# Kernel optimization log

Measured on AMD Instinct MI355X. Metric: run time of the kernel, lower is better.

The kernel has to match this reference:

```python
import jax, jax.numpy as jnp
import numpy as np

TOP_K = 4


def setup_inputs() -> dict:
    key = jax.random.key(0)
    k1, k2, k3 = jax.random.split(key, 3)
    T, H, E = 16384, 2880, 128
    hidden_states = jax.random.normal(k1, (T, H), dtype=jnp.float32)
    weight = jax.random.normal(k2, (E, H), dtype=jnp.float32) * 0.02
    bias = jax.random.normal(k3, (E,), dtype=jnp.float32) * 0.02
    return {"hidden_states": hidden_states, "weight": weight, "bias": bias}


def reference(hidden_states, weight, bias):
    # [T, H] @ [H, E] + [E] -> router logits [T, E]
    hidden_states = hidden_states.reshape(-1, weight.shape[1])
    router_logits = jnp.einsum('th,eh->te', hidden_states, weight) + bias
    # top-k over experts, then softmax over the k selected logits
    router_top_value, router_indices = jax.lax.top_k(router_logits, TOP_K)
    router_scores = jax.nn.softmax(router_top_value, axis=-1)
    return router_scores, router_indices
```

## Files before the change

### kernel.cpp

```cpp
#include <hip/hip_runtime.h>
#include <hip/hip_bf16.h>
#include <math.h>

#define T_TOKENS 16384
#define H_DIM    2880
#define KHALF    1440
#define E_EXP    128
#define TOPK     4
#define MT       32
#define MTM      64
#define KC       32
#define NCHUNK   (H_DIM / KC)
#define NCHUNK_H (KHALF / KC)
#define EPS_GAP  5e-4f

#define WS_WOFF   64
#define WS_WBYTES (NCHUNK * 1024 * 16)
#define WS_FLOFF  (WS_WOFF + WS_WBYTES)
#define WS_NEED   (WS_FLOFF + T_TOKENS * 4)

typedef __bf16 bf16x8 __attribute__((ext_vector_type(8)));
typedef float  f32x4  __attribute__((ext_vector_type(4)));

__device__ __forceinline__ void split2(float a, float b,
                                       unsigned int& hi, unsigned int& lo) {
    float2 p; p.x = a; p.y = b;
    __hip_bfloat162 h = __float22bfloat162_rn(p);
    unsigned int hu; __builtin_memcpy(&hu, &h, 4);
    float2 r;
    r.x = a - __uint_as_float((hu & 0xffffu) << 16);
    r.y = b - __uint_as_float(hu & 0xffff0000u);
    __hip_bfloat162 l = __float22bfloat162_rn(r);
    unsigned int lu; __builtin_memcpy(&lu, &l, 4);
    hi = hu; lo = lu;
}

__global__ __launch_bounds__(256) void prep_w(const float* __restrict__ W,
                                              uint4* __restrict__ wsW) {
    const int f   = blockIdx.x * 256 + threadIdx.x;
    const int kc  = f >> 9;
    const int rem = f & 511;
    const int nt  = rem >> 6;
    const int L   = rem & 63;
    const int e   = nt * 16 + (L & 15);
    const int k   = kc * KC + (L >> 4) * 8;
    const float* p = W + (size_t)e * H_DIM + k;
    const float4 x0 = *(const float4*)p;
    const float4 x1 = *(const float4*)(p + 4);
    uint4 hi, lo;
    split2(x0.x, x0.y, hi.x, lo.x);
    split2(x0.z, x0.w, hi.y, lo.y);
    split2(x1.x, x1.y, hi.z, lo.z);
    split2(x1.z, x1.w, hi.w, lo.w);
    wsW[(size_t)kc * 1024 + nt * 64 + L]       = hi;
    wsW[(size_t)kc * 1024 + 512 + nt * 64 + L] = lo;
}

__global__ __launch_bounds__(1024, 4) void router_main(
    const float* __restrict__ A, const uint4* __restrict__ wsW,
    const float* __restrict__ bias, float* __restrict__ out,
    int* __restrict__ flag_count, int* __restrict__ flag_list)
{
    union SMem {
        struct {
            uint4 W  [2][2][1024];
            uint4 Ahi[2][2][4][64];
            uint4 Alo[2][2][4][64];
        } s;
        float L[MTM][129];
    };
    __shared__ SMem sm;

    const int tid    = threadIdx.x;
    const int t_base = blockIdx.x * MTM;

    const int wave  = tid >> 6;
    const int L     = tid & 63;
    const int whalf = wave >> 3;
    const int wmg   = (wave >> 2) & 1;
    const int wng   = wave & 3;

    const int shalf = whalf;
    const int wv    = wave & 7;
    const uint4* wsrc = wsW + (size_t)(shalf * NCHUNK_H) * 1024 + (wv * 2) * 64 + L;

    const bool doA = tid < 512;
    const int at   = (tid >> 3) & 63;
    const int ac   = tid & 7;
    const int ah   = ac >> 2;
    const int akq  = ac & 3;
    const int awm  = at >> 4;
    const int aL   = (akq << 4) | (at & 15);
    const float* Ag = A + (size_t)(t_base + at) * H_DIM + ah * KHALF + akq * 8;

    f32x4 acc[2][2];
#pragma unroll
    for (int m = 0; m < 2; ++m)
#pragma unroll
        for (int n = 0; n < 2; ++n) { f32x4 z = {0.f, 0.f, 0.f, 0.f}; acc[m][n] = z; }

#define STAGE(NB, IT)                                                          \
    {                                                                          \
        if (doA) {                                                             \
            uint4 hi4, lo4;                                                    \
            split2(av0.x, av0.y, hi4.x, lo4.x);                                \
            split2(av0.z, av0.w, hi4.y, lo4.y);                                \
            split2(av1.x, av1.y, hi4.z, lo4.z);                                \
            split2(av1.z, av1.w, hi4.w, lo4.w);                                \
            sm.s.Ahi[NB][ah][awm][aL] = hi4;                                   \
            sm.s.Alo[NB][ah][awm][aL] = lo4;                                   \
        }                                                                      \
        const uint4* wc = wsrc + (size_t)(IT) * 1024;                          \
        _Pragma("unroll")                                                      \
        for (int j = 0; j < 2; ++j) {                                          \
            __builtin_amdgcn_global_load_lds(                                  \
                (const __attribute__((address_space(1))) void*)(wc + j * 64),  \
                (__attribute__((address_space(3))) void*)&sm.s.W[NB][shalf][(wv * 2 + j) * 64], \
                16, 0, 0);                                                     \
        }                                                                      \
    }

    float4 av0, av1;
    if (doA) { av0 = *(const float4*)(Ag); av1 = *(const float4*)(Ag + 4); }
    STAGE(0, 0);
    if (doA) { av0 = *(const float4*)(Ag + KC); av1 = *(const float4*)(Ag + KC + 4); }
    __syncthreads();

    int b = 0;
    for (int it = 0; it < NCHUNK_H; ++it) {
        if (it + 1 < NCHUNK_H) {
            STAGE(b ^ 1, it + 1);
            if (doA && it + 2 < NCHUNK_H) {
                av0 = *(const float4*)(Ag + (it + 2) * KC);
                av1 = *(const float4*)(Ag + (it + 2) * KC + 4);
            }
        }
        const bf16x8 ah0 = *(const bf16x8*)&sm.s.Ahi[b][whalf][wmg * 2 + 0][L];
        const bf16x8 al0 = *(const bf16x8*)&sm.s.Alo[b][whalf][wmg * 2 + 0][L];
        const bf16x8 ah1 = *(const bf16x8*)&sm.s.Ahi[b][whalf][wmg * 2 + 1][L];
        const bf16x8 al1 = *(const bf16x8*)&sm.s.Alo[b][whalf][wmg * 2 + 1][L];
#pragma unroll
        for (int n = 0; n < 2; ++n) {
            const int nt = wng * 2 + n;
            const bf16x8 whi = *(const bf16x8*)&sm.s.W[b][whalf][nt * 64 + L];
            const bf16x8 wlo = *(const bf16x8*)&sm.s.W[b][whalf][512 + nt * 64 + L];
            acc[0][n] = __builtin_amdgcn_mfma_f32_16x16x32_bf16(ah0, whi, acc[0][n], 0, 0, 0);
            acc[0][n] = __builtin_amdgcn_mfma_f32_16x16x32_bf16(ah0, wlo, acc[0][n], 0, 0, 0);
            acc[0][n] = __builtin_amdgcn_mfma_f32_16x16x32_bf16(al0, whi, acc[0][n], 0, 0, 0);
            acc[1][n] = __builtin_amdgcn_mfma_f32_16x16x32_bf16(ah1, whi, acc[1][n], 0, 0, 0);
            acc[1][n] = __builtin_amdgcn_mfma_f32_16x16x32_bf16(ah1, wlo, acc[1][n], 0, 0, 0);
            acc[1][n] = __builtin_amdgcn_mfma_f32_16x16x32_bf16(al1, whi, acc[1][n], 0, 0, 0);
        }
        __syncthreads();
        b ^= 1;
    }
#undef STAGE

    if (whalf == 0) {
#pragma unroll
        for (int m = 0; m < 2; ++m)
#pragma unroll
            for (int n = 0; n < 2; ++n) {
                const int e = (wng * 2 + n) * 16 + (L & 15);
                const float bv = bias[e];
#pragma unroll
                for (int r = 0; r < 4; ++r)
                    sm.L[(wmg * 2 + m) * 16 + (L >> 4) * 4 + r][e] = acc[m][n][r] + bv;
            }
    }
    __syncthreads();
    if (whalf == 1) {
#pragma unroll
        for (int m = 0; m < 2; ++m)
#pragma unroll
            for (int n = 0; n < 2; ++n) {
                const int e = (wng * 2 + n) * 16 + (L & 15);
#pragma unroll
                for (int r = 0; r < 4; ++r)
                    sm.L[(wmg * 2 + m) * 16 + (L >> 4) * 4 + r][e] += acc[m][n][r];
            }
    }
    __syncthreads();

    if (tid < MTM) {
        float v0 = -1e30f, v1 = -1e30f, v2 = -1e30f, v3 = -1e30f, v4 = -1e30f;
        int   i0 = 0, i1 = 0, i2 = 0, i3 = 0, i4 = 0;
        for (int e = 0; e < E_EXP; ++e) {
            const float x = sm.L[tid][e];
            if (x > v4) {
                if (x > v0)      { v4=v3;i4=i3; v3=v2;i3=i2; v2=v1;i2=i1; v1=v0;i1=i0; v0=x;i0=e; }
                else if (x > v1) { v4=v3;i4=i3; v3=v2;i3=i2; v2=v1;i2=i1; v1=x;i1=e; }
                else if (x > v2) { v4=v3;i4=i3; v3=v2;i3=i2; v2=x;i2=e; }
                else if (x > v3) { v4=v3;i4=i3; v3=x;i3=e; }
                else             { v4=x;i4=e; }
            }
        }
        const float g0 = v0 - v1, g1 = v1 - v2, g2 = v2 - v3, g3 = v3 - v4;
        float mg = g0 < g1 ? g0 : g1;
        mg = mg < g2 ? mg : g2;
        mg = mg < g3 ? mg : g3;

        const float e0x = expf(v0 - v0);
        const float e1x = expf(v1 - v0);
        const float e2x = expf(v2 - v0);
        const float e3x = expf(v3 - v0);
        const float s   = e0x + e1x + e2x + e3x;

        const int gt = t_base + tid;
        float* out_scores = out;
        float* out_idx    = out + (size_t)T_TOKENS * TOPK;
        out_scores[gt * 4 + 0] = e0x / s;
        out_scores[gt * 4 + 1] = e1x / s;
        out_scores[gt * 4 + 2] = e2x / s;
        out_scores[gt * 4 + 3] = e3x / s;
        out_idx[gt * 4 + 0] = (float)i0;
        out_idx[gt * 4 + 1] = (float)i1;
        out_idx[gt * 4 + 2] = (float)i2;
        out_idx[gt * 4 + 3] = (float)i3;

        if (mg < EPS_GAP) {
            const int p = atomicAdd(flag_count, 1);
            if (p < T_TOKENS) flag_list[p] = gt;
        }
    }
}

__global__ __launch_bounds__(512, 4) void router_main_fb(
    const float* __restrict__ A, const float* __restrict__ W,
    const float* __restrict__ bias, float* __restrict__ out,
    int* __restrict__ flag_count, int* __restrict__ flag_list)
{
    __shared__ __align__(16) uint2 sAhi[2][2][128];
    __shared__ __align__(16) uint2 sAlo[2][2][128];
    __shared__ __align__(16) uint4 sWhi[2][8][64];
    __shared__ __align__(16) uint4 sWlo[2][8][64];
    __shared__ float sL[MT][129];

    const int tid    = threadIdx.x;
    const int t_base = blockIdx.x * MT;
    const int wave  = tid >> 6;
    const int L     = tid & 63;
    const int whalf = wave >> 2;
    const int wm    = wave & 1;
    const int wn    = (wave >> 1) & 1;
    const int shalf = tid >> 8;
    const int tid_h = tid & 255;
    const int at = tid_h >> 3;
    const int ac = tid_h & 7;
    const int a_idx = (at >> 4) * 128 + ((((ac >> 1) << 4) | (at & 15)) << 1) + (ac & 1);
    const float* Ag = A + (size_t)(t_base + at) * H_DIM + shalf * KHALF + ac * 4;
    const int we  = tid_h >> 1;
    const int wq0 = (tid_h & 1) * 2;
    const float* Wg = W + (size_t)we * H_DIM + shalf * KHALF + wq0 * 8;
    const int w_nt = we >> 4;
    const int w_n  = we & 15;

    uint2* sAhiF = &sAhi[shalf][0][0];
    uint2* sAloF = &sAlo[shalf][0][0];

    f32x4 acc[4];
#pragma unroll
    for (int i = 0; i < 4; ++i) { f32x4 z = {0.f, 0.f, 0.f, 0.f}; acc[i] = z; }

    for (int k0 = 0; k0 < KHALF; k0 += KC) {
        const float4 av  = *(const float4*)(Ag + k0);
        const float4 wv0 = *(const float4*)(Wg + k0);
        const float4 wv1 = *(const float4*)(Wg + k0 + 4);
        const float4 wv2 = *(const float4*)(Wg + k0 + 8);
        const float4 wv3 = *(const float4*)(Wg + k0 + 12);

        uint2 ahp, alp;
        split2(av.x, av.y, ahp.x, alp.x);
        split2(av.z, av.w, ahp.y, alp.y);
        uint4 whp0, wlp0, whp1, wlp1;
        split2(wv0.x, wv0.y, whp0.x, wlp0.x);
        split2(wv0.z, wv0.w, whp0.y, wlp0.y);
        split2(wv1.x, wv1.y, whp0.z, wlp0.z);
        split2(wv1.z, wv1.w, whp0.w, wlp0.w);
        split2(wv2.x, wv2.y, whp1.x, wlp1.x);
        split2(wv2.z, wv2.w, whp1.y, wlp1.y);
        split2(wv3.x, wv3.y, whp1.z, wlp1.z);
        split2(wv3.z, wv3.w, whp1.w, wlp1.w);

        __syncthreads();
        sAhiF[a_idx] = ahp;
        sAloF[a_idx] = alp;
        sWhi[shalf][w_nt][((wq0 + 0) << 4) | w_n] = whp0;
        sWhi[shalf][w_nt][((wq0 + 1) << 4) | w_n] = whp1;
        sWlo[shalf][w_nt][((wq0 + 0) << 4) | w_n] = wlp0;
        sWlo[shalf][w_nt][((wq0 + 1) << 4) | w_n] = wlp1;
        __syncthreads();

        const bf16x8 ahi = *(const bf16x8*)&sAhi[whalf][wm][L * 2];
        const bf16x8 alo = *(const bf16x8*)&sAlo[whalf][wm][L * 2];
#pragma unroll
        for (int i = 0; i < 4; ++i) {
            const int nt = wn * 4 + i;
            const bf16x8 whi = *(const bf16x8*)&sWhi[whalf][nt][L];
            const bf16x8 wlo = *(const bf16x8*)&sWlo[whalf][nt][L];
            acc[i] = __builtin_amdgcn_mfma_f32_16x16x32_bf16(ahi, whi, acc[i], 0, 0, 0);
            acc[i] = __builtin_amdgcn_mfma_f32_16x16x32_bf16(ahi, wlo, acc[i], 0, 0, 0);
            acc[i] = __builtin_amdgcn_mfma_f32_16x16x32_bf16(alo, whi, acc[i], 0, 0, 0);
        }
    }

    __syncthreads();
    if (whalf == 0) {
#pragma unroll
        for (int i = 0; i < 4; ++i) {
            const int e = wn * 64 + i * 16 + (L & 15);
            const float b = bias[e];
#pragma unroll
            for (int r = 0; r < 4; ++r)
                sL[wm * 16 + (L >> 4) * 4 + r][e] = acc[i][r] + b;
        }
    }
    __syncthreads();
    if (whalf == 1) {
#pragma unroll
        for (int i = 0; i < 4; ++i) {
            const int e = wn * 64 + i * 16 + (L & 15);
#pragma unroll
            for (int r = 0; r < 4; ++r)
                sL[wm * 16 + (L >> 4) * 4 + r][e] += acc[i][r];
        }
    }
    __syncthreads();

    if (tid < MT) {
        float v0 = -1e30f, v1 = -1e30f, v2 = -1e30f, v3 = -1e30f, v4 = -1e30f;
        int   i0 = 0, i1 = 0, i2 = 0, i3 = 0, i4 = 0;
        for (int e = 0; e < E_EXP; ++e) {
            const float x = sL[tid][e];
            if (x > v4) {
                if (x > v0)      { v4=v3;i4=i3; v3=v2;i3=i2; v2=v1;i2=i1; v1=v0;i1=i0; v0=x;i0=e; }
                else if (x > v1) { v4=v3;i4=i3; v3=v2;i3=i2; v2=v1;i2=i1; v1=x;i1=e; }
                else if (x > v2) { v4=v3;i4=i3; v3=v2;i3=i2; v2=x;i2=e; }
                else if (x > v3) { v4=v3;i4=i3; v3=x;i3=e; }
                else             { v4=x;i4=e; }
            }
        }
        const float g0 = v0 - v1, g1 = v1 - v2, g2 = v2 - v3, g3 = v3 - v4;
        float mg = g0 < g1 ? g0 : g1;
        mg = mg < g2 ? mg : g2;
        mg = mg < g3 ? mg : g3;

        const float e0x = expf(v0 - v0);
        const float e1x = expf(v1 - v0);
        const float e2x = expf(v2 - v0);
        const float e3x = expf(v3 - v0);
        const float s   = e0x + e1x + e2x + e3x;

        const int gt = t_base + tid;
        float* out_scores = out;
        float* out_idx    = out + (size_t)T_TOKENS * TOPK;
        out_scores[gt * 4 + 0] = e0x / s;
        out_scores[gt * 4 + 1] = e1x / s;
        out_scores[gt * 4 + 2] = e2x / s;
        out_scores[gt * 4 + 3] = e3x / s;
        out_idx[gt * 4 + 0] = (float)i0;
        out_idx[gt * 4 + 1] = (float)i1;
        out_idx[gt * 4 + 2] = (float)i2;
        out_idx[gt * 4 + 3] = (float)i3;

        if (mg < EPS_GAP) {
            const int p = atomicAdd(flag_count, 1);
            if (p < T_TOKENS) flag_list[p] = gt;
        }
    }
}

__global__ __launch_bounds__(256) void router_recheck(
    const float* __restrict__ A, const float* __restrict__ W,
    const float* __restrict__ bias, float* __restrict__ out,
    const int* __restrict__ flag_count, const int* __restrict__ flag_list)
{
    __shared__ double sPart[256];
    __shared__ double sLog[E_EXP];

    int count = *flag_count;
    if (count > T_TOKENS) count = T_TOKENS;

    const int tid = threadIdx.x;
    const int e   = tid & (E_EXP - 1);
    const int h   = tid >> 7;

    for (int i = blockIdx.x; i < count; i += gridDim.x) {
        const int t = flag_list[i];
        const float* arow = A + (size_t)t * H_DIM + h * KHALF;
        const float* wrow = W + (size_t)e * H_DIM + h * KHALF;

        double s0 = 0.0, s1 = 0.0, s2 = 0.0, s3 = 0.0;
        float4 a[8], w[8];
#pragma unroll
        for (int q = 0; q < 8; ++q) {
            a[q] = *(const float4*)(arow + q * 4);
            w[q] = *(const float4*)(wrow + q * 4);
        }
        for (int it = 0; it < KHALF / 32 - 1; ++it) {
            const float* ap = arow + (it + 1) * 32;
            const float* wp = wrow + (it + 1) * 32;
            float4 na[8], nw[8];
#pragma unroll
            for (int q = 0; q < 8; ++q) {
                na[q] = *(const float4*)(ap + q * 4);
                nw[q] = *(const float4*)(wp + q * 4);
            }
#pragma unroll
            for (int q = 0; q < 8; ++q) {
                s0 += (double)a[q].x * (double)w[q].x;
                s1 += (double)a[q].y * (double)w[q].y;
                s2 += (double)a[q].z * (double)w[q].z;
                s3 += (double)a[q].w * (double)w[q].w;
            }
#pragma unroll
            for (int q = 0; q < 8; ++q) { a[q] = na[q]; w[q] = nw[q]; }
        }
#pragma unroll
        for (int q = 0; q < 8; ++q) {
            s0 += (double)a[q].x * (double)w[q].x;
            s1 += (double)a[q].y * (double)w[q].y;
            s2 += (double)a[q].z * (double)w[q].z;
            s3 += (double)a[q].w * (double)w[q].w;
        }
        sPart[tid] = (s0 + s1) + (s2 + s3);
        __syncthreads();
        if (h == 0) sLog[e] = sPart[e] + sPart[e + 128] + (double)bias[e];
        __syncthreads();

        if (tid == 0) {
            double v0 = -1e300, v1 = -1e300, v2 = -1e300, v3 = -1e300;
            int    i0 = 0, i1 = 0, i2 = 0, i3 = 0;
            for (int q = 0; q < E_EXP; ++q) {
                const double x = sLog[q];
                if (x > v3) {
                    if (x > v0)      { v3=v2;i3=i2; v2=v1;i2=i1; v1=v0;i1=i0; v0=x;i0=q; }
                    else if (x > v1) { v3=v2;i3=i2; v2=v1;i2=i1; v1=x;i1=q; }
                    else if (x > v2) { v3=v2;i3=i2; v2=x;i2=q; }
                    else             { v3=x;i3=q; }
                }
            }
            const double e0x = exp(v0 - v0);
            const double e1x = exp(v1 - v0);
            const double e2x = exp(v2 - v0);
            const double e3x = exp(v3 - v0);
            const double s   = e0x + e1x + e2x + e3x;
            float* out_scores = out;
            float* out_idx    = out + (size_t)T_TOKENS * TOPK;
            out_scores[t * 4 + 0] = (float)(e0x / s);
            out_scores[t * 4 + 1] = (float)(e1x / s);
            out_scores[t * 4 + 2] = (float)(e2x / s);
            out_scores[t * 4 + 3] = (float)(e3x / s);
            out_idx[t * 4 + 0] = (float)i0;
            out_idx[t * 4 + 1] = (float)i1;
            out_idx[t * 4 + 2] = (float)i2;
            out_idx[t * 4 + 3] = (float)i3;
        }
        __syncthreads();
    }
}

extern "C" void kernel_launch(void* const* d_in, const int* in_sizes, int n_in,
                              void* d_out, int out_size, void* d_ws, size_t ws_size,
                              hipStream_t stream) {
    const float* A    = (const float*)d_in[0];
    const float* W    = (const float*)d_in[1];
    const float* bias = (const float*)d_in[2];
    float* out = (float*)d_out;

    if (ws_size >= (size_t)WS_NEED) {
        int*  flag_count = (int*)d_ws;
        int*  flag_list  = (int*)((char*)d_ws + WS_FLOFF);
        uint4* wsW       = (uint4*)((char*)d_ws + WS_WOFF);
        hipMemsetAsync(flag_count, 0, sizeof(int), stream);
        prep_w<<<dim3((NCHUNK * 512) / 256), dim3(256), 0, stream>>>(W, wsW);
        router_main<<<dim3(T_TOKENS / MTM), dim3(1024), 0, stream>>>(A, wsW, bias, out,
                                                                     flag_count, flag_list);
        router_recheck<<<dim3(512), dim3(256), 0, stream>>>(A, W, bias, out,
                                                            flag_count, flag_list);
    } else {
        int* flag_count = (int*)d_ws;
        int* flag_list  = (int*)d_ws + 1;
        hipMemsetAsync(flag_count, 0, sizeof(int), stream);
        router_main_fb<<<dim3(T_TOKENS / MT), dim3(512), 0, stream>>>(A, W, bias, out,
                                                                      flag_count, flag_list);
        router_recheck<<<dim3(512), dim3(256), 0, stream>>>(A, W, bias, out,
                                                            flag_count, flag_list);
    }
}
```

Before: 374.5 us.

## Restrict fp64 recheck to near-threshold candidate experts and remap A staging

When the main kernel flags a token with a small top-k gap, it now records up to eight candidate experts whose logits lie within the gap tolerance of the fourth value. The recheck kernel then recomputes exact double-precision logits only for those candidates, and falls back to all 128 experts when there are more than eight. The token row is staged in shared memory once. The A-tile thread mapping in the main kernel is also changed so each wave writes contiguous LDS slots. The cost is a serial 128-element scan per flagged token in the main kernel's epilogue and extra workspace for the candidate list.

```diff
diff --git a/kernel.cpp b/kernel.cpp
--- a/kernel.cpp
+++ b/kernel.cpp
@@ -17,7 +17,8 @@
 #define WS_WOFF   64
 #define WS_WBYTES (NCHUNK * 1024 * 16)
 #define WS_FLOFF  (WS_WOFF + WS_WBYTES)
-#define WS_NEED   (WS_FLOFF + T_TOKENS * 4)
+#define WS_CAOFF  (WS_FLOFF + T_TOKENS * 4)
+#define WS_NEED   (WS_CAOFF + T_TOKENS * 8)
 
 typedef __bf16 bf16x8 __attribute__((ext_vector_type(8)));
 typedef float  f32x4  __attribute__((ext_vector_type(4)));
@@ -59,7 +60,8 @@
 __global__ __launch_bounds__(1024, 4) void router_main(
     const float* __restrict__ A, const uint4* __restrict__ wsW,
     const float* __restrict__ bias, float* __restrict__ out,
-    int* __restrict__ flag_count, int* __restrict__ flag_list)
+    int* __restrict__ flag_count, int* __restrict__ flag_list,
+    uint2* __restrict__ cand_list)
 {
     union SMem {
         struct {
@@ -85,12 +87,11 @@
     const uint4* wsrc = wsW + (size_t)(shalf * NCHUNK_H) * 1024 + (wv * 2) * 64 + L;
 
     const bool doA = tid < 512;
-    const int at   = (tid >> 3) & 63;
-    const int ac   = tid & 7;
-    const int ah   = ac >> 2;
-    const int akq  = ac & 3;
-    const int awm  = at >> 4;
-    const int aL   = (akq << 4) | (at & 15);
+    const int ah   = wave & 1;
+    const int awm  = (wave >> 1) & 3;
+    const int akq  = L >> 4;
+    const int t16  = L & 15;
+    const int at   = awm * 16 + t16;
     const float* Ag = A + (size_t)(t_base + at) * H_DIM + ah * KHALF + akq * 8;
 
     f32x4 acc[2][2];
@@ -107,8 +108,8 @@
             split2(av0.z, av0.w, hi4.y, lo4.y);                                \
             split2(av1.x, av1.y, hi4.z, lo4.z);                                \
             split2(av1.z, av1.w, hi4.w, lo4.w);                                \
-            sm.s.Ahi[NB][ah][awm][aL] = hi4;                                   \
-            sm.s.Alo[NB][ah][awm][aL] = lo4;                                   \
+            sm.s.Ahi[NB][ah][awm][L] = hi4;                                    \
+            sm.s.Alo[NB][ah][awm][L] = lo4;                                    \
         }                                                                      \
         const uint4* wc = wsrc + (size_t)(IT) * 1024;                          \
         _Pragma("unroll")                                                      \
@@ -220,8 +221,150 @@
 
         if (mg < EPS_GAP) {
             const int p = atomicAdd(flag_count, 1);
-            if (p < T_TOKENS) flag_list[p] = gt;
-        }
+            if (p < T_TOKENS) {
+                flag_list[p] = gt;
+                unsigned ids[8];
+                int nc = 0;
+                const float thr = v3 - EPS_GAP;
+                for (int e = 0; e < E_EXP; ++e) {
+                    if (sm.L[tid][e] >= thr) {
+                        if (nc < 8) ids[nc] = (unsigned)e;
+                        ++nc;
+                    }
+                }
+                uint2 cd;
+                if (nc > 8) {
+                    cd.x = 0xFEu; cd.y = 0xFFFFFFFFu;
+                } else {
+                    for (int q = nc; q < 8; ++q) ids[q] = 0xFFu;
+                    cd.x = ids[0] | (ids[1] << 8) | (ids[2] << 16) | (ids[3] << 24);
+                    cd.y = ids[4] | (ids[5] << 8) | (ids[6] << 16) | (ids[7] << 24);
+                }
+                cand_list[p] = cd;
+            }
+        }
+    }
+}
+
+__global__ __launch_bounds__(256) void router_recheck(
+    const float* __restrict__ A, const float* __restrict__ W,
+    const float* __restrict__ bias, float* __restrict__ out,
+    const int* __restrict__ flag_count, const int* __restrict__ flag_list,
+    const uint2* __restrict__ cand_list)
+{
+    __shared__ float  sA[H_DIM];
+    __shared__ double sLog[8];
+    __shared__ int    sIds[8];
+    __shared__ double sPart[256];
+    __shared__ double sFull[E_EXP];
+
+    int count = *flag_count;
+    if (count > T_TOKENS) count = T_TOKENS;
+
+    const int tid = threadIdx.x;
+
+    for (int i = blockIdx.x; i < count; i += gridDim.x) {
+        const int t = flag_list[i];
+        const uint2 cd = cand_list[i];
+        __syncthreads();
+
+        for (int q = tid; q < H_DIM / 4; q += 256)
+            *(float4*)&sA[q * 4] = *(const float4*)(A + (size_t)t * H_DIM + q * 4);
+        __syncthreads();
+
+        const bool full = ((cd.x & 0xFFu) == 0xFEu);
+        if (!full) {
+            const int sl = tid >> 5;
+            const int j  = tid & 31;
+            const unsigned e = (sl < 4 ? (cd.x >> (sl * 8)) : (cd.y >> ((sl - 4) * 8))) & 0xFFu;
+            double sum = 0.0;
+            if (e < E_EXP) {
+                const float* wrow = W + (size_t)e * H_DIM;
+                for (int k = j; k < H_DIM; k += 32)
+                    sum += (double)sA[k] * (double)wrow[k];
+            }
+#pragma unroll
+            for (int off = 16; off > 0; off >>= 1)
+                sum += __shfl_down(sum, off, 32);
+            if (j == 0) {
+                sIds[sl] = (e < E_EXP) ? (int)e : -1;
+                sLog[sl] = (e < E_EXP) ? (sum + (double)bias[e]) : -1e300;
+            }
+            __syncthreads();
+            if (tid == 0) {
+                double v0 = -1e300, v1 = -1e300, v2 = -1e300, v3 = -1e300;
+                int    i0 = 0, i1 = 0, i2 = 0, i3 = 0;
+                for (int q = 0; q < 8; ++q) {
+                    if (sIds[q] < 0) continue;
+                    const double x = sLog[q];
+                    const int    id = sIds[q];
+                    if (x > v3) {
+                        if (x > v0)      { v3=v2;i3=i2; v2=v1;i2=i1; v1=v0;i1=i0; v0=x;i0=id; }
+                        else if (x > v1) { v3=v2;i3=i2; v2=v1;i2=i1; v1=x;i1=id; }
+                        else if (x > v2) { v3=v2;i3=i2; v2=x;i2=id; }
+                        else             { v3=x;i3=id; }
+                    }
+                }
+                const double e0x = exp(v0 - v0);
+                const double e1x = exp(v1 - v0);
+                const double e2x = exp(v2 - v0);
+                const double e3x = exp(v3 - v0);
+                const double s   = e0x + e1x + e2x + e3x;
+                float* out_scores = out;
+                float* out_idx    = out + (size_t)T_TOKENS * TOPK;
+                out_scores[t * 4 + 0] = (float)(e0x / s);
+                out_scores[t * 4 + 1] = (float)(e1x / s);
+                out_scores[t * 4 + 2] = (float)(e2x / s);
+                out_scores[t * 4 + 3] = (float)(e3x / s);
+                out_idx[t * 4 + 0] = (float)i0;
+                out_idx[t * 4 + 1] = (float)i1;
+                out_idx[t * 4 + 2] = (float)i2;
+                out_idx[t * 4 + 3] = (float)i3;
+            }
+        } else {
+            const int e = tid & (E_EXP - 1);
+            const int h = tid >> 7;
+            const float* wrow = W + (size_t)e * H_DIM + h * KHALF;
+            const float* arow = &sA[h * KHALF];
+            double s0 = 0.0, s1 = 0.0;
+            for (int k = 0; k < KHALF; k += 2) {
+                s0 += (double)arow[k]     * (double)wrow[k];
+                s1 += (double)arow[k + 1] * (double)wrow[k + 1];
+            }
+            sPart[tid] = s0 + s1;
+            __syncthreads();
+            if (h == 0) sFull[e] = sPart[e] + sPart[e + 128] + (double)bias[e];
+            __syncthreads();
+            if (tid == 0) {
+                double v0 = -1e300, v1 = -1e300, v2 = -1e300, v3 = -1e300;
+                int    i0 = 0, i1 = 0, i2 = 0, i3 = 0;
+                for (int q = 0; q < E_EXP; ++q) {
+                    const double x = sFull[q];
+                    if (x > v3) {
+                        if (x > v0)      { v3=v2;i3=i2; v2=v1;i2=i1; v1=v0;i1=i0; v0=x;i0=q; }
+                        else if (x > v1) { v3=v2;i3=i2; v2=v1;i2=i1; v1=x;i1=q; }
+                        else if (x > v2) { v3=v2;i3=i2; v2=x;i2=q; }
+                        else             { v3=x;i3=q; }
+                    }
+                }
+                const double e0x = exp(v0 - v0);
+                const double e1x = exp(v1 - v0);
+                const double e2x = exp(v2 - v0);
+                const double e3x = exp(v3 - v0);
+                const double s   = e0x + e1x + e2x + e3x;
+                float* out_scores = out;
+                float* out_idx    = out + (size_t)T_TOKENS * TOPK;
+                out_scores[t * 4 + 0] = (float)(e0x / s);
+                out_scores[t * 4 + 1] = (float)(e1x / s);
+                out_scores[t * 4 + 2] = (float)(e2x / s);
+                out_scores[t * 4 + 3] = (float)(e3x / s);
+                out_idx[t * 4 + 0] = (float)i0;
+                out_idx[t * 4 + 1] = (float)i1;
+                out_idx[t * 4 + 2] = (float)i2;
+                out_idx[t * 4 + 3] = (float)i3;
+            }
+        }
+        __syncthreads();
     }
 }
 
@@ -370,7 +513,7 @@
     }
 }
 
-__global__ __launch_bounds__(256) void router_recheck(
+__global__ __launch_bounds__(256) void router_recheck_fb(
     const float* __restrict__ A, const float* __restrict__ W,
     const float* __restrict__ bias, float* __restrict__ out,
     const int* __restrict__ flag_count, const int* __restrict__ flag_list)
@@ -469,22 +612,23 @@
     float* out = (float*)d_out;
 
     if (ws_size >= (size_t)WS_NEED) {
-        int*  flag_count = (int*)d_ws;
-        int*  flag_list  = (int*)((char*)d_ws + WS_FLOFF);
-        uint4* wsW       = (uint4*)((char*)d_ws + WS_WOFF);
+        int*   flag_count = (int*)d_ws;
+        uint4* wsW        = (uint4*)((char*)d_ws + WS_WOFF);
+        int*   flag_list  = (int*)((char*)d_ws + WS_FLOFF);
+        uint2* cand_list  = (uint2*)((char*)d_ws + WS_CAOFF);
         hipMemsetAsync(flag_count, 0, sizeof(int), stream);
         prep_w<<<dim3((NCHUNK * 512) / 256), dim3(256), 0, stream>>>(W, wsW);
-        router_main<<<dim3(T_TOKENS / MTM), dim3(1024), 0, stream>>>(A, wsW, bias, out,
-                                                                     flag_count, flag_list);
-        router_recheck<<<dim3(512), dim3(256), 0, stream>>>(A, W, bias, out,
-                                                            flag_count, flag_list);
+        router_main<<<dim3(T_TOKENS / MTM), dim3(1024), 0, stream>>>(
+            A, wsW, bias, out, flag_count, flag_list, cand_list);
+        router_recheck<<<dim3(512), dim3(256), 0, stream>>>(
+            A, W, bias, out, flag_count, flag_list, cand_list);
     } else {
         int* flag_count = (int*)d_ws;
         int* flag_list  = (int*)d_ws + 1;
         hipMemsetAsync(flag_count, 0, sizeof(int), stream);
         router_main_fb<<<dim3(T_TOKENS / MT), dim3(512), 0, stream>>>(A, W, bias, out,
                                                                       flag_count, flag_list);
-        router_recheck<<<dim3(512), dim3(256), 0, stream>>>(A, W, bias, out,
-                                                            flag_count, flag_list);
+        router_recheck_fb<<<dim3(512), dim3(256), 0, stream>>>(A, W, bias, out,
+                                                               flag_count, flag_list);
     }
 }
```

Measured after the change: 354.9 us. 1.06x faster.
